# Kernel optimization log

Measured on AMD Instinct MI355X. Metric: run time of the kernel, lower is better.

## Reference

```python
import jax, jax.numpy as jnp
import numpy as np
from jax import lax

H, W = 1024, 2048
WIN = (3, 3)            # eps=1.5 on the integer grid == 8-neighborhood (3x3 window)
MIN_SAMPLES = 4         # sklearn DBSCAN counts the point itself
MIN_CLUSTER = 30        # clusters smaller than this become noise
N_SLOTS = 26            # output channels
INT32_MAX = np.iinfo(np.int32).max


def setup_inputs() -> dict:
    key = jax.random.key(0)
    mask = jax.random.normal(key, (H, W), dtype=jnp.float32)
    return {"mask": mask}


def _minpool(x):
    # 3x3 min over int32 labels, SAME padding with +inf identity
    return lax.reduce_window(x, INT32_MAX, lax.min, WIN, (1, 1), 'SAME')


def _forward(mask):
    h, w = mask.shape
    hw = h * w
    BIG = jnp.int32(hw)  # sentinel label for 'not in any cluster'

    active = mask > 0.1
    # neighbor count in 3x3 (includes self) -> DBSCAN core condition
    cnt = lax.reduce_window(active.astype(jnp.int32), 0, lax.add, WIN, (1, 1), 'SAME')
    core = active & (cnt >= MIN_SAMPLES)

    idx2d = jnp.arange(hw, dtype=jnp.int32).reshape(h, w)
    L0 = jnp.where(core, idx2d, BIG)

    # connected components over core pixels: min-label hook (3x3 min-pool)
    # + pointer jumping (path compression) until fixpoint
    def body(st):
        L, _ = st
        Ln = jnp.where(core, jnp.minimum(L, _minpool(L)), BIG)
        flat = Ln.ravel()
        table = jnp.concatenate([flat, jnp.array([hw], jnp.int32)])  # BIG -> BIG
        flat = table[table[flat]]  # two pointer-jump hops
        Ln = flat.reshape(h, w)
        return Ln, jnp.all(Ln == L)

    def cond(st):
        return jnp.logical_not(st[1])

    L, _ = lax.while_loop(cond, body, (L0, jnp.array(False)))

    # border points: active non-core pixels with a core neighbor join the
    # (deterministically min-labeled) neighboring core cluster
    pooled = _minpool(L)
    final = jnp.where(core, L, jnp.where(active & (pooled < BIG), pooled, BIG))

    flatL = final.ravel()
    labeled = flatL < BIG
    ids = jnp.where(labeled, flatL, hw)  # noise -> extra bucket hw

    sizes = jax.ops.segment_sum(labeled.astype(jnp.int32), ids, num_segments=hw + 1)[:hw]
    col = jnp.broadcast_to(jnp.arange(w, dtype=jnp.float32), (h, w)).ravel()
    colsum = jax.ops.segment_sum(jnp.where(labeled, col, 0.0), ids, num_segments=hw + 1)[:hw]

    valid = sizes >= MIN_CLUSTER  # size filter (loc.sum() < 30 -> noise)
    means = jnp.where(valid, colsum / jnp.maximum(sizes, 1), jnp.inf)
    order = jnp.argsort(means)  # valid clusters first, sorted by mean column
    rank = jnp.zeros(hw, jnp.int32).at[order].set(jnp.arange(hw, dtype=jnp.int32))

    lab = jnp.where(labeled, flatL, 0)
    ch = rank[lab]
    pix_ok = labeled & valid[lab] & (ch < N_SLOTS)
    ch2d = jnp.where(pix_ok, ch, N_SLOTS).reshape(h, w)  # N_SLOTS == 'no channel'
    # scatter 1s into the rank-th channel
    return (ch2d[None] == jnp.arange(N_SLOTS, dtype=jnp.int32)[:, None, None]).astype(jnp.uint8)


def reference(mask):
    return _forward(mask)
```

## Files before the change

kernel.cpp:

```cpp
#include <hip/hip_runtime.h>
#include <stdint.h>

#define HH 1024
#define WW 2048
#define HWN (HH*WW)
#define BIGL HWN
#define NSLOTS 26
#define MINCL 30
#define THREADS 256
#define LTHREADS 512
#define MAXCAND 70000
#define HSZ 512
#define TILE 4096
#define NTILES 512
#define NB 128

typedef int vi4 __attribute__((ext_vector_type(4)));

__device__ __forceinline__ int uf_load(int* p, int i) {
    return __hip_atomic_load(&p[i], __ATOMIC_RELAXED, __HIP_MEMORY_SCOPE_AGENT);
}
__device__ __forceinline__ void uf_store(int* p, int i, int v) {
    __hip_atomic_store(&p[i], v, __ATOMIC_RELAXED, __HIP_MEMORY_SCOPE_AGENT);
}
__device__ int uf_find(int* parent, int x) {
    int p = uf_load(parent, x);
    while (p != x) {
        int gp = uf_load(parent, p);
        if (gp != p) uf_store(parent, x, gp);
        x = p; p = gp;
    }
    return p;
}
__device__ void uf_union(int* parent, int a, int b) {
    int ra = uf_find(parent, a);
    int rb = uf_find(parent, b);
    while (ra != rb) {
        if (ra > rb) { int t = ra; ra = rb; rb = t; }
        int old = atomicCAS(&parent[rb], rb, ra);
        if (old == rb) return;
        rb = uf_find(parent, old);
        ra = uf_find(parent, ra);
    }
}

__device__ __forceinline__ int l_load(int* p, int i) {
    return __hip_atomic_load(&p[i], __ATOMIC_RELAXED, __HIP_MEMORY_SCOPE_WORKGROUP);
}
__device__ __forceinline__ void l_store(int* p, int i, int v) {
    __hip_atomic_store(&p[i], v, __ATOMIC_RELAXED, __HIP_MEMORY_SCOPE_WORKGROUP);
}
__device__ int l_find(int* lp, int x) {
    int p = l_load(lp, x);
    while (p != x) {
        int gp = l_load(lp, p);
        if (gp != p) l_store(lp, x, gp);
        x = p; p = gp;
    }
    return p;
}
__device__ void l_union(int* lp, int a, int b) {
    int ra = l_find(lp, a);
    int rb = l_find(lp, b);
    while (ra != rb) {
        if (ra > rb) { int t = ra; ra = rb; rb = t; }
        int old = atomicCAS(&lp[rb], rb, ra);
        if (old == rb) return;
        rb = l_find(lp, old);
        ra = l_find(lp, ra);
    }
}

__global__ __launch_bounds__(LTHREADS) void k_local(const float* __restrict__ mask,
                                                    uint8_t* __restrict__ flags,
                                                    int* __restrict__ parent,
                                                    int* __restrict__ sizes,
                                                    unsigned long long* __restrict__ colsum,
                                                    signed char* __restrict__ chan,
                                                    int* __restrict__ counter) {
    __shared__ uint8_t lact[66 * 72];
    __shared__ uint8_t lc8[TILE];
    __shared__ int lp[TILE];
    const int tid = threadIdx.x;
    int tile_x = blockIdx.x & 31, tile_y = blockIdx.x >> 5;
    int r0 = tile_y << 6, c0 = tile_x << 6;

    {
        int base = blockIdx.x * (HWN / NTILES);
        vi4* sz4 = (vi4*)(sizes + base);
        vi4* cs4 = (vi4*)(colsum + base);
        for (int t = tid; t < 1024; t += LTHREADS) sz4[t] = (vi4)0;
        for (int t = tid; t < 2048; t += LTHREADS) cs4[t] = (vi4)0;
        vi4* ch4 = (vi4*)(chan + base);
        for (int t = tid; t < 256; t += LTHREADS) ch4[t] = (vi4)(-1);
        if (blockIdx.x == 0 && tid == 0) *counter = 0;
    }

    {
        int tx = tid & 15, ty = tid >> 4;
        for (int yy = ty; yy < 66; yy += 32) {
            int gr = r0 - 1 + yy;
            for (int xx = tx; xx < 66; xx += 16) {
                int gc = c0 - 1 + xx;
                bool a = false;
                if ((unsigned)gr < HH && (unsigned)gc < WW)
                    a = mask[gr * WW + gc] > 0.1f;
                lact[yy * 72 + xx] = a ? 1 : 0;
            }
        }
    }
    __syncthreads();
    for (int li = tid; li < TILE; li += LTHREADS) {
        int lr = li >> 6, lc = li & 63;
        int b = (lr + 1) * 72 + (lc + 1);
        int a = lact[b];
        int cnt = lact[b - 73] + lact[b - 72] + lact[b - 71]
                + lact[b - 1]  + a           + lact[b + 1]
                + lact[b + 71] + lact[b + 72] + lact[b + 73];
        lc8[li] = (uint8_t)(a | ((a && cnt >= 4) ? 2 : 0));
        lp[li] = li;
    }
    __syncthreads();
    if (tid < 256) {
        int row = tid >> 2, chunk = tid & 3;
        ((uint4*)(flags + (size_t)(r0 + row) * WW + c0))[chunk] =
            ((const uint4*)lc8)[row * 4 + chunk];
    }
    for (int li = tid; li < TILE; li += LTHREADS) {
        if (!(lc8[li] & 2)) continue;
        int lr = li >> 6, lc = li & 63;
        if (lc > 0 && (lc8[li - 1] & 2)) l_union(lp, li, li - 1);
        if (lr > 0) {
            if (lc > 0  && (lc8[li - 65] & 2)) l_union(lp, li, li - 65);
            if (           (lc8[li - 64] & 2)) l_union(lp, li, li - 64);
            if (lc < 63 && (lc8[li - 63] & 2)) l_union(lp, li, li - 63);
        }
    }
    __syncthreads();
    for (int li = tid; li < TILE; li += LTHREADS) {
        if (!(lc8[li] & 2)) continue;
        int root = li, p;
        while ((p = lp[root]) != root) root = p;
        int gi = (r0 + (li >> 6)) * WW + c0 + (li & 63);
        int gr = (r0 + (root >> 6)) * WW + c0 + (root & 63);
        parent[gi] = gr;
    }
}

__global__ __launch_bounds__(THREADS) void k_merge(const uint8_t* __restrict__ flags,
                                                   int* __restrict__ parent) {
    int tile_x = blockIdx.x & 31, tile_y = blockIdx.x >> 5;
    int r0 = tile_y << 6, c0 = tile_x << 6;
    int t = threadIdx.x;
    int lane = t & 63;

    if (t < 64) {
        int r = r0, c = c0 + t, i = r * WW + c;
        bool selfC = (flags[i] & 2) != 0;
        bool nC = false, nwC = false, neC = false;
        if (selfC && r > 0) {
            nC  = (flags[i - WW] & 2) != 0;
            nwC = (c > 0)      && (flags[i - WW - 1] & 2);
            neC = (c < WW - 1) && (flags[i - WW + 1] & 2);
        }
        int did = 0, ra = -1, rb = -1;
        if (selfC && r > 0 && nC) { ra = uf_find(parent, i); rb = uf_find(parent, i - WW); did = 1; }
        int pra = __shfl_up(ra, 1), prb = __shfl_up(rb, 1), pdid = __shfl_up(did, 1);
        bool head = (lane == 0) || !pdid || pra != ra || prb != rb;
        if (did && head) uf_union(parent, ra, rb);
        if (selfC && r > 0) {
            if (t == 0) {
                if (nwC) uf_union(parent, i, i - WW - 1);
                if (!nC && neC) uf_union(parent, i, i - WW + 1);
            } else if (t == 63) {
                if (!nC && nwC) uf_union(parent, i, i - WW - 1);
                if (neC) {
                    bool eC = (c < WW - 1) && (flags[i + 1] & 2);
                    if (!eC) uf_union(parent, i, i - WW + 1);
                }
            } else if (!nC) {
                if (nwC) uf_union(parent, i, i - WW - 1);
                if (neC) uf_union(parent, i, i - WW + 1);
            }
        }
        if (t == 0 && selfC && c > 0 && (flags[i - 1] & 2))
            uf_union(parent, i, i - 1);
    } else if (t < 127) {
        int lr = t - 63;
        int r = r0 + lr, c = c0, i = r * WW + c;
        bool selfC = (flags[i] & 2) != 0;
        bool wC = false, nwC = false;
        if (selfC && c > 0) {
            wC  = (flags[i - 1] & 2) != 0;
            nwC = (flags[i - WW - 1] & 2) != 0;
        }
        int did = 0, ra = -1, rb = -1;
        if (selfC && wC) { ra = uf_find(parent, i); rb = uf_find(parent, i - 1); did = 1; }
        int pra = __shfl_up(ra, 1), prb = __shfl_up(rb, 1), pdid = __shfl_up(did, 1);
        bool head = (lane == 0) || !pdid || pra != ra || prb != rb;
        if (did && head) uf_union(parent, ra, rb);
        if (selfC && !wC && nwC) uf_union(parent, i, i - WW - 1);
    } else if (t < 190) {
        int lr = t - 126;
        int r = r0 + lr, c = c0 + 63, i = r * WW + c;
        bool selfC = (flags[i] & 2) != 0;
        if (selfC && c < WW - 1) {
            bool neC = (flags[i - WW + 1] & 2) != 0;
            bool eC  = (flags[i + 1] & 2) != 0;
            if (neC && !eC) uf_union(parent, i, i - WW + 1);
        }
    }
}

__global__ __launch_bounds__(THREADS) void k_border_stats(
        const uint8_t* __restrict__ flags, int* __restrict__ parent,
        int* __restrict__ labfull, int* __restrict__ sizes,
        unsigned long long* __restrict__ colsum,
        int* __restrict__ cand, int* __restrict__ counter) {
    __shared__ int h_lab[HSZ];
    __shared__ int h_sz[HSZ];
    __shared__ unsigned long long h_cs[HSZ];
    for (int t = threadIdx.x; t < HSZ; t += THREADS) {
        h_lab[t] = -1; h_sz[t] = 0; h_cs[t] = 0;
    }
    __syncthreads();

    int i = blockIdx.x * THREADS + threadIdx.x;
    int f = flags[i];
    int lab = BIGL;
    if (f & 2) {
        lab = uf_find(parent, i);
    } else if (f & 1) {
        int r = i >> 11, c = i & (WW - 1);
        int m = BIGL;
        #pragma unroll
        for (int dr = -1; dr <= 1; ++dr) {
            int rr = r + dr;
            if (rr < 0 || rr >= HH) continue;
            #pragma unroll
            for (int dc = -1; dc <= 1; ++dc) {
                int cc = c + dc;
                if (cc < 0 || cc >= WW) continue;
                int n = rr * WW + cc;
                if (flags[n] & 2) {
                    int v = uf_find(parent, n);
                    if (v < m) m = v;
                }
            }
        }
        lab = m;
    }
    labfull[i] = lab;

    int lane = threadIdx.x & 63;
    int labp = __shfl_up(lab, 1);
    bool head = (lane == 0) || (labp != lab);
    unsigned long long hm = __ballot(head);
    if (head && lab < BIGL) {
        unsigned long long rest = (hm >> lane) >> 1;
        int len = rest ? __ffsll((unsigned long long)rest) : (64 - lane);
        long long c0 = (long long)(i & (WW - 1));
        unsigned long long csum =
            (unsigned long long)(c0 * len + (long long)len * (len - 1) / 2);
        unsigned slot = (((unsigned)lab * 2654435761u) >> 20) & (HSZ - 1);
        for (;;) {
            int old = atomicCAS(&h_lab[slot], -1, lab);
            if (old == -1 || old == lab) {
                atomicAdd(&h_sz[slot], len);
                atomicAdd(&h_cs[slot], csum);
                break;
            }
            slot = (slot + 1) & (HSZ - 1);
        }
    }
    __syncthreads();
    for (int t = threadIdx.x; t < HSZ; t += THREADS) {
        int lb = h_lab[t];
        if (lb >= 0) {
            int add = h_sz[t];
            int old = atomicAdd(&sizes[lb], add);
            if (old < MINCL && old + add >= MINCL) {
                int p = atomicAdd(counter, 1);
                cand[p] = lb;
            }
            atomicAdd(&colsum[lb], h_cs[t]);
        }
    }
}

__global__ __launch_bounds__(THREADS) void k_sel1(const int* __restrict__ cand,
                                                  const int* __restrict__ counter,
                                                  const int* __restrict__ sizes,
                                                  const unsigned long long* __restrict__ colsum,
                                                  unsigned long long* __restrict__ top26g) {
    __shared__ unsigned long long keys[1024];
    __shared__ unsigned long long skey[THREADS];
    __shared__ int sidx[THREADS];
    const int tid = threadIdx.x;
    int n = *counter;
    int slice = (n + NB - 1) / NB;
    if (slice > 1024) slice = 1024;
    int j0 = blockIdx.x * slice;
    int j1 = j0 + slice; if (j1 > n) j1 = n;
    int len = j1 - j0; if (len < 0) len = 0;
    for (int t = tid; t < len; t += THREADS) {
        int lab = cand[j0 + t];
        float mean = (float)colsum[lab] / (float)sizes[lab];
        keys[t] = ((unsigned long long)__float_as_uint(mean) << 32) | (unsigned int)lab;
    }
    __syncthreads();
    for (int k = 0; k < NSLOTS; ++k) {
        unsigned long long lk = ~0ull; int li = -1;
        for (int t = tid; t < len; t += THREADS)
            if (keys[t] < lk) { lk = keys[t]; li = t; }
        skey[tid] = lk; sidx[tid] = li;
        __syncthreads();
        for (int s = THREADS / 2; s > 0; s >>= 1) {
            if (tid < s && skey[tid + s] < skey[tid]) {
                skey[tid] = skey[tid + s]; sidx[tid] = sidx[tid + s];
            }
            __syncthreads();
        }
        if (tid == 0) {
            unsigned long long best = skey[0];
            top26g[blockIdx.x * NSLOTS + k] = best;
            if (best != ~0ull) keys[sidx[0]] = ~0ull;
        }
        __syncthreads();
    }
}

__global__ __launch_bounds__(1024) void k_sel2(const unsigned long long* __restrict__ top26g,
                                               signed char* __restrict__ chan) {
    __shared__ unsigned long long keys[NB * NSLOTS];
    __shared__ unsigned long long skey[1024];
    __shared__ int sidx[1024];
    const int tid = threadIdx.x;
    const int NK = NB * NSLOTS;
    for (int t = tid; t < NK; t += 1024) keys[t] = top26g[t];
    __syncthreads();
    for (int k = 0; k < NSLOTS; ++k) {
        unsigned long long lk = ~0ull; int li = -1;
        for (int t = tid; t < NK; t += 1024)
            if (keys[t] < lk) { lk = keys[t]; li = t; }
        skey[tid] = lk; sidx[tid] = li;
        __syncthreads();
        for (int s = 512; s > 0; s >>= 1) {
            if (tid < s && skey[tid + s] < skey[tid]) {
                skey[tid] = skey[tid + s]; sidx[tid] = sidx[tid + s];
            }
            __syncthreads();
        }
        if (tid == 0) {
            unsigned long long best = skey[0];
            if (best != ~0ull) {
                chan[(unsigned int)(best & 0xFFFFFFFFull)] = (signed char)k;
                keys[sidx[0]] = ~0ull;
            }
        }
        __syncthreads();
    }
}

__global__ __launch_bounds__(THREADS) void k_output(const int* __restrict__ labfull,
                                                    const signed char* __restrict__ chan,
                                                    int* __restrict__ out) {
    int i4 = (blockIdx.x * THREADS + threadIdx.x) * 4;
    int chv[4];
    #pragma unroll
    for (int t = 0; t < 4; ++t) {
        int lab = labfull[i4 + t];
        chv[t] = (lab < BIGL) ? (int)chan[lab] : -1;
    }
    #pragma unroll
    for (int c = 0; c < NSLOTS; ++c) {
        vi4 v;
        v.x = (chv[0] == c) ? 1 : 0;
        v.y = (chv[1] == c) ? 1 : 0;
        v.z = (chv[2] == c) ? 1 : 0;
        v.w = (chv[3] == c) ? 1 : 0;
        __builtin_nontemporal_store(v, (vi4*)(out + (size_t)c * HWN + i4));
    }
}

extern "C" void kernel_launch(void* const* d_in, const int* in_sizes, int n_in,
                              void* d_out, int out_size, void* d_ws, size_t ws_size,
                              hipStream_t stream) {
    const float* mask = (const float*)d_in[0];
    int* out = (int*)d_out;

    char* w = (char*)d_ws;
    int* parent                 = (int*)(w);
    int* labfull                = (int*)(w + (size_t)HWN * 4);
    int* sizes                  = (int*)(w + (size_t)HWN * 8);
    unsigned long long* colsum  = (unsigned long long*)(w + (size_t)HWN * 12);
    uint8_t* flags              = (uint8_t*)(w + (size_t)HWN * 20);
    signed char* chan           = (signed char*)(w + (size_t)HWN * 21);
    int* cand                   = (int*)(w + (size_t)HWN * 22);
    int* counter                = (int*)(w + (size_t)HWN * 22 + MAXCAND * 4);
    unsigned long long* top26g  = (unsigned long long*)(w + (size_t)HWN * 22 + MAXCAND * 4 + 256);

    const int blocks = HWN / THREADS;
    k_local       <<<NTILES, LTHREADS, 0, stream>>>(mask, flags, parent,
                                                    sizes, colsum, chan, counter);
    k_merge       <<<NTILES, THREADS, 0, stream>>>(flags, parent);
    k_border_stats<<<blocks, THREADS, 0, stream>>>(flags, parent, labfull, sizes, colsum,
                                                   cand, counter);
    k_sel1        <<<NB, THREADS, 0, stream>>>(cand, counter, sizes, colsum, top26g);
    k_sel2        <<<1, 1024, 0, stream>>>(top26g, chan);
    k_output      <<<HWN / (4 * THREADS), THREADS, 0, stream>>>(labfull, chan, out);
}
```

Measured before the change: 416.0 us.

## Fuse top-26 selection kernels with last-block reduction and wave-shuffle minima

Merges the two selection kernels into one: each block keeps its candidate keys in registers and repeatedly extracts the minimum with wave shuffles instead of shared-memory tree reductions full of barriers. The last block to finish, detected with an atomic counter, performs the global top-26 merge and writes channel assignments, which removes a kernel launch and a serial single-block pass. The register layout handles at most 768 candidates per block (3 per lane across 4 waves), so larger candidate counts would be silently dropped. Duplicate keys are impossible because labels are unique, so the per-lane removal by equality is safe.

Result: faster. 405.4 us (-2.6%).

```diff
diff --git a/kernel.cpp b/kernel.cpp
--- a/kernel.cpp
+++ b/kernel.cpp
@@ -16,6 +16,7 @@
 #define NB 128
 
 typedef int vi4 __attribute__((ext_vector_type(4)));
+typedef unsigned long long u64;
 
 __device__ __forceinline__ int uf_load(int* p, int i) {
     return __hip_atomic_load(&p[i], __ATOMIC_RELAXED, __HIP_MEMORY_SCOPE_AGENT);
@@ -93,7 +94,7 @@
         for (int t = tid; t < 2048; t += LTHREADS) cs4[t] = (vi4)0;
         vi4* ch4 = (vi4*)(chan + base);
         for (int t = tid; t < 256; t += LTHREADS) ch4[t] = (vi4)(-1);
-        if (blockIdx.x == 0 && tid == 0) *counter = 0;
+        if (blockIdx.x == 0 && tid == 0) { counter[0] = 0; counter[1] = 0; }
     }
 
     {
@@ -288,77 +289,99 @@
     }
 }
 
-__global__ __launch_bounds__(THREADS) void k_sel1(const int* __restrict__ cand,
-                                                  const int* __restrict__ counter,
-                                                  const int* __restrict__ sizes,
-                                                  const unsigned long long* __restrict__ colsum,
-                                                  unsigned long long* __restrict__ top26g) {
-    __shared__ unsigned long long keys[1024];
-    __shared__ unsigned long long skey[THREADS];
-    __shared__ int sidx[THREADS];
-    const int tid = threadIdx.x;
-    int n = *counter;
+__device__ __forceinline__ u64 wave_min_u64(u64 m) {
+    #pragma unroll
+    for (int off = 32; off; off >>= 1) {
+        u64 o = __shfl_xor(m, off);
+        if (o < m) m = o;
+    }
+    return m;
+}
+
+__global__ __launch_bounds__(THREADS) void k_sel(const int* __restrict__ cand,
+                                                 int* __restrict__ counter,
+                                                 const int* __restrict__ sizes,
+                                                 const unsigned long long* __restrict__ colsum,
+                                                 unsigned long long* __restrict__ top26g,
+                                                 signed char* __restrict__ chan) {
+    __shared__ u64 wout[4 * NSLOTS];
+    const int tid = threadIdx.x, lane = tid & 63, wv = tid >> 6;
+    const int n = counter[0];
     int slice = (n + NB - 1) / NB;
-    if (slice > 1024) slice = 1024;
     int j0 = blockIdx.x * slice;
     int j1 = j0 + slice; if (j1 > n) j1 = n;
     int len = j1 - j0; if (len < 0) len = 0;
-    for (int t = tid; t < len; t += THREADS) {
-        int lab = cand[j0 + t];
-        float mean = (float)colsum[lab] / (float)sizes[lab];
-        keys[t] = ((unsigned long long)__float_as_uint(mean) << 32) | (unsigned int)lab;
-    }
-    __syncthreads();
+    int chunk = (len + 3) >> 2;
+    int s0 = j0 + wv * chunk;
+    int s1 = s0 + chunk; if (s1 > j1) s1 = j1;
+
+    u64 kk[3] = { ~0ull, ~0ull, ~0ull };
+    #pragma unroll
+    for (int t = 0; t < 3; ++t) {
+        int j = s0 + lane + 64 * t;
+        if (j < s1) {
+            int lab = cand[j];
+            float mean = (float)colsum[lab] / (float)sizes[lab];
+            kk[t] = ((u64)__float_as_uint(mean) << 32) | (unsigned)lab;
+        }
+    }
     for (int k = 0; k < NSLOTS; ++k) {
-        unsigned long long lk = ~0ull; int li = -1;
-        for (int t = tid; t < len; t += THREADS)
-            if (keys[t] < lk) { lk = keys[t]; li = t; }
-        skey[tid] = lk; sidx[tid] = li;
-        __syncthreads();
-        for (int s = THREADS / 2; s > 0; s >>= 1) {
-            if (tid < s && skey[tid + s] < skey[tid]) {
-                skey[tid] = skey[tid + s]; sidx[tid] = sidx[tid + s];
-            }
-            __syncthreads();
-        }
-        if (tid == 0) {
-            unsigned long long best = skey[0];
-            top26g[blockIdx.x * NSLOTS + k] = best;
-            if (best != ~0ull) keys[sidx[0]] = ~0ull;
-        }
-        __syncthreads();
-    }
-}
-
-__global__ __launch_bounds__(1024) void k_sel2(const unsigned long long* __restrict__ top26g,
-                                               signed char* __restrict__ chan) {
-    __shared__ unsigned long long keys[NB * NSLOTS];
-    __shared__ unsigned long long skey[1024];
-    __shared__ int sidx[1024];
-    const int tid = threadIdx.x;
-    const int NK = NB * NSLOTS;
-    for (int t = tid; t < NK; t += 1024) keys[t] = top26g[t];
-    __syncthreads();
+        u64 m = kk[0]; int li = 0;
+        if (kk[1] < m) { m = kk[1]; li = 1; }
+        if (kk[2] < m) { m = kk[2]; li = 2; }
+        u64 mpre = m;
+        m = wave_min_u64(m);
+        if (mpre == m && m != ~0ull) kk[li] = ~0ull;
+        if (lane == 0) wout[wv * NSLOTS + k] = m;
+    }
+    __syncthreads();
+    if (wv == 0) {
+        u64 a = (lane < 4 * NSLOTS) ? wout[lane] : ~0ull;
+        u64 b = (lane + 64 < 4 * NSLOTS) ? wout[lane + 64] : ~0ull;
+        for (int k = 0; k < NSLOTS; ++k) {
+            u64 m = a < b ? a : b; int li = a < b ? 0 : 1;
+            u64 mpre = m;
+            m = wave_min_u64(m);
+            if (mpre == m && m != ~0ull) { if (li == 0) a = ~0ull; else b = ~0ull; }
+            if (lane == 0) top26g[blockIdx.x * NSLOTS + k] = m;
+        }
+    }
+    __syncthreads();
+    __shared__ int lastflag;
+    if (tid == 0) {
+        __threadfence();
+        lastflag = (atomicAdd(&counter[1], 1) == NB - 1);
+    }
+    __syncthreads();
+    if (!lastflag) return;
+
+    u64 mk[13];
+    #pragma unroll
+    for (int t = 0; t < 13; ++t) {
+        int j = wv * 832 + lane + 64 * t;
+        mk[t] = __hip_atomic_load(&top26g[j], __ATOMIC_RELAXED, __HIP_MEMORY_SCOPE_AGENT);
+    }
     for (int k = 0; k < NSLOTS; ++k) {
-        unsigned long long lk = ~0ull; int li = -1;
-        for (int t = tid; t < NK; t += 1024)
-            if (keys[t] < lk) { lk = keys[t]; li = t; }
-        skey[tid] = lk; sidx[tid] = li;
-        __syncthreads();
-        for (int s = 512; s > 0; s >>= 1) {
-            if (tid < s && skey[tid + s] < skey[tid]) {
-                skey[tid] = skey[tid + s]; sidx[tid] = sidx[tid + s];
-            }
-            __syncthreads();
-        }
-        if (tid == 0) {
-            unsigned long long best = skey[0];
-            if (best != ~0ull) {
-                chan[(unsigned int)(best & 0xFFFFFFFFull)] = (signed char)k;
-                keys[sidx[0]] = ~0ull;
-            }
-        }
-        __syncthreads();
+        u64 m = mk[0]; int li = 0;
+        #pragma unroll
+        for (int t = 1; t < 13; ++t) if (mk[t] < m) { m = mk[t]; li = t; }
+        u64 mpre = m;
+        m = wave_min_u64(m);
+        if (mpre == m && m != ~0ull) mk[li] = ~0ull;
+        if (lane == 0) wout[wv * NSLOTS + k] = m;
+    }
+    __syncthreads();
+    if (wv == 0) {
+        u64 a = (lane < 4 * NSLOTS) ? wout[lane] : ~0ull;
+        u64 b = (lane + 64 < 4 * NSLOTS) ? wout[lane + 64] : ~0ull;
+        for (int k = 0; k < NSLOTS; ++k) {
+            u64 m = a < b ? a : b; int li = a < b ? 0 : 1;
+            u64 mpre = m;
+            m = wave_min_u64(m);
+            if (mpre == m && m != ~0ull) { if (li == 0) a = ~0ull; else b = ~0ull; }
+            if (lane == 0 && m != ~0ull)
+                chan[(unsigned int)(m & 0xFFFFFFFFull)] = (signed char)k;
+        }
     }
 }
 
@@ -406,7 +429,6 @@
     k_merge       <<<NTILES, THREADS, 0, stream>>>(flags, parent);
     k_border_stats<<<blocks, THREADS, 0, stream>>>(flags, parent, labfull, sizes, colsum,
                                                    cand, counter);
-    k_sel1        <<<NB, THREADS, 0, stream>>>(cand, counter, sizes, colsum, top26g);
-    k_sel2        <<<1, 1024, 0, stream>>>(top26g, chan);
+    k_sel         <<<NB, THREADS, 0, stream>>>(cand, counter, sizes, colsum, top26g, chan);
     k_output      <<<HWN / (4 * THREADS), THREADS, 0, stream>>>(labfull, chan, out);
 }
```
